# Performance work log

Measured on AMD Instinct MI355X. Metric: run time of the kernel, lower is better.

The kernel has to match this reference:

```python
import jax, jax.numpy as jnp
import numpy as np

N = 50000      # nodes
E = 800000     # edges (avg degree 16)
F_IN = 128
H = 128        # hidden_channels
C = 10         # num_classes
S = 5          # Chebyshev order K
B = 8          # graphs in batch


def setup_inputs() -> dict:
    key = jax.random.key(0)
    ks = jax.random.split(key, 9)
    x = jax.random.normal(ks[0], (N, F_IN), jnp.float32)
    edge_index = jax.random.randint(ks[1], (2, E), 0, N, dtype=jnp.int64)
    batch = jnp.sort(jax.random.randint(ks[2], (N,), 0, B, dtype=jnp.int64))
    lambda_max = 2.0 * jnp.ones((B,), jnp.float32)
    W1 = jax.random.normal(ks[3], (S, F_IN, H), jnp.float32) * 0.05
    b1 = jax.random.normal(ks[4], (H,), jnp.float32) * 0.05
    W2 = jax.random.normal(ks[5], (S, H, H), jnp.float32) * 0.05
    b2 = jax.random.normal(ks[6], (H,), jnp.float32) * 0.05
    Wlin = jax.random.normal(ks[7], (H, C), jnp.float32) * 0.05
    blin = jax.random.normal(ks[8], (C,), jnp.float32) * 0.05
    return {"x": x, "edge_index": edge_index, "batch": batch,
            "lambda_max": lambda_max, "W1": W1, "b1": b1,
            "W2": W2, "b2": b2, "Wlin": Wlin, "blin": blin}


def _cheb_conv(x, row, col, w_edge, diag, W, b):
    # scaled Laplacian matvec: L_hat v = scatter(w_edge * v[col] -> row) + diag * v
    def Lhat(v):
        msg = v[col] * w_edge[:, None]                       # [E, d]
        return jax.ops.segment_sum(msg, row, num_segments=N) + diag[:, None] * v

    Tx0 = x
    out = Tx0 @ W[0]
    Tx1 = Lhat(Tx0)
    out = out + Tx1 @ W[1]
    for k in range(2, W.shape[0]):                           # Chebyshev recurrence
        Tx2 = 2.0 * Lhat(Tx1) - Tx0
        out = out + Tx2 @ W[k]
        Tx0, Tx1 = Tx1, Tx2
    return out + b


def reference(x, edge_index, batch, lambda_max, W1, b1, W2, b2, Wlin, blin):
    row, col = edge_index[0], edge_index[1]
    # sym-normalized Laplacian L = I - D^{-1/2} A D^{-1/2}; L_hat = 2L/lambda_max - I
    deg = jax.ops.segment_sum(jnp.ones((E,), x.dtype), row, num_segments=N)
    dis = jnp.where(deg > 0, jax.lax.rsqrt(jnp.maximum(deg, 1e-12)), 0.0)
    lam_e = lambda_max[batch[row]]                           # per-edge lambda_max
    w_edge = -2.0 * dis[row] * dis[col] / lam_e              # off-diagonal of L_hat
    diag = 2.0 / lambda_max[batch] - 1.0                     # diagonal of L_hat per node

    h = jax.nn.relu(_cheb_conv(x, row, col, w_edge, diag, W1, b1))
    h = jax.nn.relu(_cheb_conv(h, row, col, w_edge, diag, W2, b2))

    # global_mean_pool over batch assignment
    sums = jax.ops.segment_sum(h, batch, num_segments=B)     # [B, H]
    counts = jax.ops.segment_sum(jnp.ones((N, 1), h.dtype), batch, num_segments=B)
    pooled = sums / jnp.maximum(counts, 1.0)
    return pooled @ Wlin + blin                              # [B, C] logits (softmax unused in forward)
```

## Files before the change

kernel.cpp:

```cpp
#include <hip/hip_runtime.h>
#include <hip/hip_bf16.h>
#include <stdint.h>

typedef __attribute__((ext_vector_type(8))) short bf16x8;
typedef __attribute__((ext_vector_type(4))) float f32x4;

__device__ __forceinline__ float bf16lo_to_f(uint32_t u) { return __uint_as_float(u << 16); }
__device__ __forceinline__ float bf16hi_to_f(uint32_t u) { return __uint_as_float(u & 0xffff0000u); }
__device__ __forceinline__ uint16_t f_to_bf16(float f) {
    uint32_t u = __float_as_uint(f);
    uint32_t r = u + 0x7fff + ((u >> 16) & 1);
    return (uint16_t)(r >> 16);
}


#define BINCH 4096

__global__ void __launch_bounds__(256) k_bhist(const int* __restrict__ row,
                                               int* __restrict__ bhist, int E) {
    __shared__ int sh[256];
    int t = threadIdx.x;
    sh[t] = 0;
    __syncthreads();
    int stride = gridDim.x * blockDim.x;
    for (int e = blockIdx.x * blockDim.x + t; e < E; e += stride)
        atomicAdd(&sh[row[e] >> 8], 1);
    __syncthreads();
    if (sh[t]) atomicAdd(&bhist[t], sh[t]);
}

__global__ void k_bscan(const int* __restrict__ bhist, int* __restrict__ gbase,
                        int* __restrict__ gcur, float* __restrict__ mS, int nbk, int N) {
    __shared__ int sh[256];
    int t = threadIdx.x;
    int v = t < nbk ? bhist[t] : 0;
    sh[t] = v;
    __syncthreads();
    for (int o = 1; o < 256; o <<= 1) {
        int u = (t >= o) ? sh[t - o] : 0;
        __syncthreads();
        sh[t] += u;
        __syncthreads();
    }
    gbase[t] = sh[t] - v;
    gcur[t] = sh[t] - v;
    if (t == 255) gbase[256] = sh[255];
    if (t < 5) mS[(size_t)t * (N + 1) + N] = 0.f;
}

__global__ void __launch_bounds__(256) k_bin(const int* __restrict__ row,
        const int* __restrict__ col, int* __restrict__ gcur,
        uint32_t* __restrict__ bout, int E) {
    __shared__ uint32_t stage[BINCH];
    __shared__ int hist[256], hscan[256], hcur[256], gofs[256];
    int t = threadIdx.x;
    int e0 = blockIdx.x * BINCH;
    int ecnt = min(BINCH, E - e0);
    hist[t] = 0;
    __syncthreads();
    for (int i = t; i < ecnt; i += 256)
        atomicAdd(&hist[row[e0 + i] >> 8], 1);
    __syncthreads();
    int v = hist[t];
    hscan[t] = v;
    __syncthreads();
    for (int o = 1; o < 256; o <<= 1) {
        int u = (t >= o) ? hscan[t - o] : 0;
        __syncthreads();
        hscan[t] += u;
        __syncthreads();
    }
    hcur[t] = hscan[t] - v;
    __syncthreads();
    for (int i = t; i < ecnt; i += 256) {
        int r = row[e0 + i];
        int p = atomicAdd(&hcur[r >> 8], 1);
        stage[p] = (uint32_t)(r & 255) | ((uint32_t)col[e0 + i] << 8);
    }
    __syncthreads();
    if (v > 0) gofs[t] = atomicAdd(&gcur[t], v);
    __syncthreads();
    for (int i = t; i < ecnt; i += 256) {
        int lo = 0, hi = 255;
        while (lo < hi) { int mid = (lo + hi) >> 1; if (hscan[mid] > i) hi = mid; else lo = mid + 1; }
        int b = lo;
        int local = i - (hscan[b] - hist[b]);
        bout[gofs[b] + local] = stage[i];
    }
}

__global__ void __launch_bounds__(256) k_deg2(const uint32_t* __restrict__ bout,
        const int* __restrict__ gbase, int* __restrict__ deg,
        int* __restrict__ psum, int N) {
    __shared__ int cnt[256];
    __shared__ int red[256];
    int t = threadIdx.x, b = blockIdx.x;
    cnt[t] = 0;
    __syncthreads();
    int s = gbase[b], epos = gbase[b + 1];
    for (int i = s + t; i < epos; i += 256)
        atomicAdd(&cnt[bout[i] & 255], 1);
    __syncthreads();
    int n = b * 256 + t;
    int d = cnt[t];
    if (n < N) deg[n] = d;
    red[t] = (n < N) ? ((d + 7) & ~7) : 0;
    __syncthreads();
    for (int o = 128; o > 0; o >>= 1) {
        if (t < o) red[t] += red[t + o];
        __syncthreads();
    }
    if (t == 0) psum[b] = red[0];
}

__global__ void k_scanp(const int* __restrict__ psum, int* __restrict__ poff,
                        int* __restrict__ offs, int nb, int N) {
    __shared__ int sh[256];
    int t = threadIdx.x;
    int per = (nb + 255) >> 8;
    int base = t * per;
    int s = 0;
    for (int i = 0; i < per; i++) { int idx = base + i; if (idx < nb) s += psum[idx]; }
    sh[t] = s;
    __syncthreads();
    for (int o = 1; o < 256; o <<= 1) {
        int u = (t >= o) ? sh[t - o] : 0;
        __syncthreads();
        sh[t] += u;
        __syncthreads();
    }
    int run = sh[t] - s;
    for (int i = 0; i < per; i++) {
        int idx = base + i;
        if (idx < nb) { poff[idx] = run; run += psum[idx]; }
    }
    if (t == 255) offs[N] = sh[255];
}

__global__ void k_offs(const int* __restrict__ deg, const int* __restrict__ poff,
                       int* __restrict__ offs,
                       const int* __restrict__ batch, const float* __restrict__ lam,
                       float* __restrict__ dis, float* __restrict__ diag, int N) {
    __shared__ int sh[256];
    int t = threadIdx.x;
    int idx = blockIdx.x * 256 + t;
    int d = idx < N ? deg[idx] : 0;
    int v = (d + 7) & ~7;
    sh[t] = v;
    __syncthreads();
    for (int o = 1; o < 256; o <<= 1) {
        int u = (t >= o) ? sh[t - o] : 0;
        __syncthreads();
        sh[t] += u;
        __syncthreads();
    }
    if (idx < N) {
        offs[idx] = poff[blockIdx.x] + sh[t] - v;
        dis[idx] = d > 0 ? rsqrtf((float)d) : 0.f;
        diag[idx] = 2.f / lam[batch[idx]] - 1.f;
    }
}

__global__ void __launch_bounds__(256) k_csr2(const uint32_t* __restrict__ bout,
        const int* __restrict__ gbase, const int* __restrict__ offs,
        uint16_t* __restrict__ csr, int N) {
    __shared__ int cur[256];
    int t = threadIdx.x, b = blockIdx.x;
    int n = b * 256 + t;
    int o0 = n < N ? offs[n] : 0;
    cur[t] = o0;
    __syncthreads();
    int s = gbase[b], epos = gbase[b + 1];
    for (int i = s + t; i < epos; i += 256) {
        uint32_t v = bout[i];
        int p = atomicAdd(&cur[v & 255], 1);
        csr[p] = (uint16_t)(v >> 8);
    }
    __syncthreads();
    if (n < N) {
        int e = cur[t];
        int pe = o0 + ((e - o0 + 7) & ~7);
        for (int p = e; p < pe; p++) csr[p] = (uint16_t)N;
    }
}

__global__ void k_prepw(const float* __restrict__ W1, uint16_t* __restrict__ Wt1,
                        const float* __restrict__ W2, uint16_t* __restrict__ Wt2) {
    int i = blockIdx.x * blockDim.x + threadIdx.x;
    const float* W = W1; uint16_t* Wt = Wt1;
    if (i >= 128 * 640) { i -= 128 * 640; W = W2; Wt = Wt2; }
    int o = i / 640, kk = i % 640;
    Wt[(size_t)o * 640 + kk] = f_to_bf16(W[(size_t)kk * 128 + o]);
}

__global__ void __launch_bounds__(256) k_castx(const float* __restrict__ x,
        uint16_t* __restrict__ Txb, int8_t* __restrict__ Txq,
        const float* __restrict__ dis, float* __restrict__ mS,
        float* __restrict__ scq, int N) {
    int n = (blockIdx.x * blockDim.x + threadIdx.x) >> 6;
    int lane = threadIdx.x & 63;
    if (n >= N) return;
    float2 v = ((const float2*)x)[(size_t)n * 64 + lane];
    uint32_t p = (uint32_t)f_to_bf16(v.x) | ((uint32_t)f_to_bf16(v.y) << 16);
    __builtin_nontemporal_store(p, &((uint32_t*)Txb)[(size_t)n * 320 + lane]);
    float m = fmaxf(fabsf(v.x), fabsf(v.y));
    for (int o = 1; o < 64; o <<= 1) m = fmaxf(m, __shfl_xor(m, o));
    float inv = m > 0.f ? 127.f / m : 0.f;
    int qx = (int)rintf(v.x * inv), qy = (int)rintf(v.y * inv);
    uint16_t qp = (uint16_t)((qx & 0xff) | ((qy & 0xff) << 8));
    *(uint16_t*)(Txq + (size_t)n * 640 + 2 * lane) = qp;
    if (lane == 0) {
        float sc = m > 0.f ? m * (1.f / 127.f) : 0.f;
        mS[n] = sc * dis[n];
        scq[n] = sc;
    }
}

__global__ void __launch_bounds__(256) k_lhat(
        int8_t* __restrict__ Txq, uint16_t* __restrict__ Txb,
        const int* __restrict__ offs, const uint16_t* __restrict__ csr,
        const float* __restrict__ diag, const float* __restrict__ dis,
        float* __restrict__ mS, float* __restrict__ scq, int N,
        int src, int dst, int prev, float alpha, int use_prev) {
    int n = (blockIdx.x * blockDim.x + threadIdx.x) >> 6;
    int lane = threadIdx.x & 63;
    if (n >= N) return;
    int beg = offs[n], end = offs[n + 1];
    float dgn = diag[n], dn = dis[n];
    float aS = -alpha * dn * (dgn + 1.0f);
    const float* mSrc = mS + (size_t)src * (N + 1);
    const int8_t* qbase = Txq + src * 128 + 2 * lane;
    float ax = 0.f, ay = 0.f;
    for (int e = beg; e < end; e += 8) {
        uint4 cw = *(const uint4*)(csr + e);
        int cc[8] = { (int)(cw.x & 0xffff), (int)(cw.x >> 16),
                      (int)(cw.y & 0xffff), (int)(cw.y >> 16),
                      (int)(cw.z & 0xffff), (int)(cw.z >> 16),
                      (int)(cw.w & 0xffff), (int)(cw.w >> 16) };
        float mm[8];
        uint16_t qv[8];
#pragma unroll
        for (int u = 0; u < 8; u++) mm[u] = mSrc[cc[u]];
#pragma unroll
        for (int u = 0; u < 8; u++)
            qv[u] = *(const uint16_t*)(qbase + (size_t)cc[u] * 640);
#pragma unroll
        for (int u = 0; u < 8; u++) {
            float f = aS * mm[u];
            ax = fmaf(f, (float)(int)(int8_t)(qv[u] & 0xff), ax);
            ay = fmaf(f, (float)(int)(int8_t)(qv[u] >> 8), ay);
        }
    }
    {
        uint16_t qsv = *(const uint16_t*)(Txq + (size_t)n * 640 + src * 128 + 2 * lane);
        float ad = alpha * dgn * scq[(size_t)src * (N + 1) + n];
        ax = fmaf(ad, (float)(int)(int8_t)(qsv & 0xff), ax);
        ay = fmaf(ad, (float)(int)(int8_t)(qsv >> 8), ay);
    }
    if (use_prev) {
        uint16_t qpv = *(const uint16_t*)(Txq + (size_t)n * 640 + prev * 128 + 2 * lane);
        float sp = scq[(size_t)prev * (N + 1) + n];
        ax = fmaf(-sp, (float)(int)(int8_t)(qpv & 0xff), ax);
        ay = fmaf(-sp, (float)(int)(int8_t)(qpv >> 8), ay);
    }
    uint32_t outv = (uint32_t)f_to_bf16(ax) | ((uint32_t)f_to_bf16(ay) << 16);
    __builtin_nontemporal_store(outv, &((uint32_t*)Txb)[(size_t)n * 320 + dst * 64 + lane]);
    float m = fmaxf(fabsf(ax), fabsf(ay));
    for (int o = 1; o < 64; o <<= 1) m = fmaxf(m, __shfl_xor(m, o));
    float inv = m > 0.f ? 127.f / m : 0.f;
    int qx = (int)rintf(ax * inv), qy = (int)rintf(ay * inv);
    uint16_t qp = (uint16_t)((qx & 0xff) | ((qy & 0xff) << 8));
    *(uint16_t*)(Txq + (size_t)n * 640 + dst * 128 + 2 * lane) = qp;
    if (lane == 0) {
        float sc = m > 0.f ? m * (1.f / 127.f) : 0.f;
        mS[(size_t)dst * (N + 1) + n] = sc * dn;
        scq[(size_t)dst * (N + 1) + n] = sc;
    }
}

#define BM 128
#define BK 64
#define LDT 72
#define LDC 132

__global__ void __launch_bounds__(256) k_gemm(
        const uint16_t* __restrict__ A, int lda,
        const uint16_t* __restrict__ Bt,
        const float* __restrict__ bias,
        uint16_t* __restrict__ out, int ldo,
        uint16_t* __restrict__ out2b,
        int8_t* __restrict__ out2q,
        const float* __restrict__ dis, float* __restrict__ mS,
        float* __restrict__ scq,
        int M, int Kdim) {
    __shared__ uint16_t smem[BM * LDT + 128 * LDT];
    uint16_t* As = smem;
    uint16_t* Bs = smem + BM * LDT;
    uint16_t* Ct = smem;
    int t = threadIdx.x;
    int w = t >> 6, lane = t & 63;
    int row0 = blockIdx.x * BM;
    int mrow = (w >> 1) * 64, ncol = (w & 1) * 64;

    int ar[4], akc[4];
#pragma unroll
    for (int rep = 0; rep < 4; rep++) {
        int d = rep * 256 + t;
        ar[rep] = d >> 3; akc[rep] = d & 7;
    }

    f32x4 acc[4][4];
#pragma unroll
    for (int i = 0; i < 4; i++)
#pragma unroll
        for (int j = 0; j < 4; j++) acc[i][j] = (f32x4){0.f, 0.f, 0.f, 0.f};

    bf16x8 pa[4], pb[4];
#pragma unroll
    for (int rep = 0; rep < 4; rep++) {
        int grow = row0 + ar[rep];
        bf16x8 va = {0, 0, 0, 0, 0, 0, 0, 0};
        if (grow < M) va = *(const bf16x8*)(A + (size_t)grow * lda + akc[rep] * 8);
        pa[rep] = va;
        pb[rep] = *(const bf16x8*)(Bt + (size_t)ar[rep] * Kdim + akc[rep] * 8);
    }

    for (int k0 = 0; k0 < Kdim; k0 += BK) {
#pragma unroll
        for (int rep = 0; rep < 4; rep++) {
            *(bf16x8*)(&As[ar[rep] * LDT + akc[rep] * 8]) = pa[rep];
            *(bf16x8*)(&Bs[ar[rep] * LDT + akc[rep] * 8]) = pb[rep];
        }
        __syncthreads();
        int kn = k0 + BK;
        if (kn < Kdim) {
#pragma unroll
            for (int rep = 0; rep < 4; rep++) {
                int grow = row0 + ar[rep];
                bf16x8 va = {0, 0, 0, 0, 0, 0, 0, 0};
                if (grow < M) va = *(const bf16x8*)(A + (size_t)grow * lda + kn + akc[rep] * 8);
                pa[rep] = va;
                pb[rep] = *(const bf16x8*)(Bt + (size_t)ar[rep] * Kdim + kn + akc[rep] * 8);
            }
        }
#pragma unroll
        for (int ks = 0; ks < BK; ks += 32) {
            bf16x8 af[4], bfr[4];
#pragma unroll
            for (int i = 0; i < 4; i++) {
                int r = mrow + i * 16 + (lane & 15);
                af[i] = *(const bf16x8*)(&As[r * LDT + ks + (lane >> 4) * 8]);
            }
#pragma unroll
            for (int j = 0; j < 4; j++) {
                int c = ncol + j * 16 + (lane & 15);
                bfr[j] = *(const bf16x8*)(&Bs[c * LDT + ks + (lane >> 4) * 8]);
            }
#pragma unroll
            for (int i = 0; i < 4; i++)
#pragma unroll
                for (int j = 0; j < 4; j++)
                    acc[i][j] = __builtin_amdgcn_mfma_f32_16x16x32_bf16(af[i], bfr[j], acc[i][j], 0, 0, 0);
        }
        __syncthreads();
    }

#pragma unroll
    for (int j = 0; j < 4; j++) {
        int c = ncol + j * 16 + (lane & 15);
        float bv = bias[c];
#pragma unroll
        for (int i = 0; i < 4; i++) {
            int rloc = mrow + i * 16 + (lane >> 4) * 4;
#pragma unroll
            for (int r = 0; r < 4; r++) {
                float v = acc[i][j][r] + bv;
                v = v > 0.f ? v : 0.f;
                Ct[(rloc + r) * LDC + c] = f_to_bf16(v);
            }
        }
    }
    __syncthreads();
#pragma unroll
    for (int rep = 0; rep < 8; rep++) {
        int d = rep * 256 + t;
        int r = d >> 4, c8 = (d & 15) * 8;
        int grow = row0 + r;
        if (grow < M) {
            bf16x8 v = *(const bf16x8*)(&Ct[r * LDC + c8]);
            if (out)   *(bf16x8*)(out + (size_t)grow * ldo + c8) = v;
            if (out2b) *(bf16x8*)(out2b + (size_t)grow * 640 + c8) = v;
        }
    }
    if (out2q) {
        int r = t >> 1, half = t & 1;
        int grow = row0 + r;
        float vmax = 0.f;
        for (int j = 0; j < 32; j++) {
            uint32_t u = *(const uint32_t*)(&Ct[r * LDC + half * 64 + j * 2]);
            vmax = fmaxf(vmax, fmaxf(fabsf(bf16lo_to_f(u)), fabsf(bf16hi_to_f(u))));
        }
        vmax = fmaxf(vmax, __shfl_xor(vmax, 1));
        if (grow < M) {
            float inv = vmax > 0.f ? 127.f / vmax : 0.f;
            for (int j0 = 0; j0 < 16; j0++) {
                uint32_t u0 = *(const uint32_t*)(&Ct[r * LDC + half * 64 + j0 * 4]);
                uint32_t u1 = *(const uint32_t*)(&Ct[r * LDC + half * 64 + j0 * 4 + 2]);
                int q0 = (int)rintf(bf16lo_to_f(u0) * inv);
                int q1 = (int)rintf(bf16hi_to_f(u0) * inv);
                int q2 = (int)rintf(bf16lo_to_f(u1) * inv);
                int q3 = (int)rintf(bf16hi_to_f(u1) * inv);
                uint32_t pk = (q0 & 0xff) | ((q1 & 0xff) << 8) |
                              ((q2 & 0xff) << 16) | ((uint32_t)(q3 & 0xff) << 24);
                *(uint32_t*)(out2q + (size_t)grow * 640 + half * 64 + j0 * 4) = pk;
            }
            if (half == 0) {
                float sc = vmax > 0.f ? vmax * (1.f / 127.f) : 0.f;
                mS[grow] = sc * dis[grow];
                scq[grow] = sc;
            }
        }
    }
}

__global__ void __launch_bounds__(128) k_pool(const uint16_t* __restrict__ h,
        const int* __restrict__ batch, float* __restrict__ pooled, int N, int CH) {
    int f = threadIdx.x;
    int n0 = blockIdx.x * CH;
    if (n0 >= N) return;
    int n1 = min(n0 + CH, N);
    float acc = 0.f;
    int cur = batch[n0];
    for (int n = n0; n < n1; ++n) {
        int b = batch[n];
        if (b != cur) { atomicAdd(&pooled[cur * 128 + f], acc); acc = 0.f; cur = b; }
        acc += __uint_as_float(((uint32_t)h[(size_t)n * 128 + f]) << 16);
    }
    atomicAdd(&pooled[cur * 128 + f], acc);
}

__global__ void k_final(const float* __restrict__ pooled, const int* __restrict__ batch,
                        const float* __restrict__ Wlin, const float* __restrict__ blin,
                        float* __restrict__ out, int N, int B_, int C_) {
    __shared__ int cnt[64];
    int t = threadIdx.x;
    if (t < B_) {
        auto lb = [&](int v) {
            int lo = 0, hi = N;
            while (lo < hi) {
                int mid = (lo + hi) >> 1;
                if (batch[mid] < v) lo = mid + 1; else hi = mid;
            }
            return lo;
        };
        cnt[t] = lb(t + 1) - lb(t);
    }
    __syncthreads();
    if (t < B_ * C_) {
        int b = t / C_, c = t % C_;
        float inv = 1.f / fmaxf((float)cnt[b], 1.f);
        float acc = blin[c];
        for (int f = 0; f < 128; ++f) acc += pooled[b * 128 + f] * inv * Wlin[f * C_ + c];
        out[t] = acc;
    }
}

extern "C" void kernel_launch(void* const* d_in, const int* in_sizes, int n_in,
                              void* d_out, int out_size, void* d_ws, size_t ws_size,
                              hipStream_t stream) {
    const float* x    = (const float*)d_in[0];
    const int*   edge = (const int*)d_in[1];
    const int*   batch= (const int*)d_in[2];
    const float* lam  = (const float*)d_in[3];
    const float* W1   = (const float*)d_in[4];
    const float* b1   = (const float*)d_in[5];
    const float* W2   = (const float*)d_in[6];
    const float* b2   = (const float*)d_in[7];
    const float* Wlin = (const float*)d_in[8];
    const float* blin = (const float*)d_in[9];
    const int E  = in_sizes[1] / 2;
    const int N  = in_sizes[2];
    const int B_ = in_sizes[3];
    const int* row = edge;
    const int* col = edge + E;

    char* ws = (char*)d_ws;
    size_t off = 0;
    auto take = [&](size_t bytes) -> char* {
        char* p = ws + off;
        off = (off + bytes + 255) & ~(size_t)255;
        return p;
    };
    uint16_t* Txb    = (uint16_t*)take((size_t)N * 640 * 2);
    int8_t*   Txq    = (int8_t*)take((size_t)(N + 1) * 640);
    uint16_t* h      = (uint16_t*)take((size_t)N * 128 * 2);
    uint16_t* csr    = (uint16_t*)take(((size_t)E + 8 * (size_t)N) * 2);
    uint32_t* bout   = (uint32_t*)take((size_t)E * 4);
    float*    mS     = (float*)take((size_t)5 * (N + 1) * 4);
    float*    scq    = (float*)take((size_t)5 * (N + 1) * 4);
    int*      deg    = (int*)take((size_t)N * 4);
    int*      offs   = (int*)take((size_t)(N + 1) * 4);
    float*    dis    = (float*)take((size_t)N * 4);
    float*    diag   = (float*)take((size_t)N * 4);
    uint16_t* Wt1    = (uint16_t*)take((size_t)128 * 640 * 2);
    uint16_t* Wt2    = (uint16_t*)take((size_t)128 * 640 * 2);
    float*    pooled = (float*)take((size_t)B_ * 128 * 4);
    int*      bhist  = (int*)take(257 * 4);
    int*      gbase  = (int*)take(257 * 4);
    int*      gcur   = (int*)take(257 * 4);
    const int nb = (N + 255) / 256;
    int*      psum   = (int*)take((size_t)nb * 4);
    int*      poff   = (int*)take((size_t)nb * 4);

    hipMemsetAsync(pooled, 0, (size_t)B_ * 128 * 4, stream);
    hipMemsetAsync(bhist, 0, 257 * 4, stream);

    k_bhist<<<112, 256, 0, stream>>>(row, bhist, E);
    k_bscan<<<1, 256, 0, stream>>>(bhist, gbase, gcur, mS, nb, N);
    k_bin<<<(E + BINCH - 1) / BINCH, 256, 0, stream>>>(row, col, gcur, bout, E);
    k_deg2<<<nb, 256, 0, stream>>>(bout, gbase, deg, psum, N);
    k_scanp<<<1, 256, 0, stream>>>(psum, poff, offs, nb, N);
    k_offs<<<nb, 256, 0, stream>>>(deg, poff, offs, batch, lam, dis, diag, N);
    k_csr2<<<nb, 256, 0, stream>>>(bout, gbase, offs, csr, N);
    k_prepw<<<(2 * 128 * 640) / 256, 256, 0, stream>>>(W1, Wt1, W2, Wt2);
    k_castx<<<(N + 3) / 4, 256, 0, stream>>>(x, Txb, Txq, dis, mS, scq, N);

    const int lblocks = (N + 3) / 4;
    const int gblocks = (N + BM - 1) / BM;

    k_lhat<<<lblocks, 256, 0, stream>>>(Txq, Txb, offs, csr, diag, dis, mS, scq, N, 0, 1, 0, 1.f, 0);
    k_lhat<<<lblocks, 256, 0, stream>>>(Txq, Txb, offs, csr, diag, dis, mS, scq, N, 1, 2, 0, 2.f, 1);
    k_lhat<<<lblocks, 256, 0, stream>>>(Txq, Txb, offs, csr, diag, dis, mS, scq, N, 2, 3, 1, 2.f, 1);
    k_lhat<<<lblocks, 256, 0, stream>>>(Txq, Txb, offs, csr, diag, dis, mS, scq, N, 3, 4, 2, 2.f, 1);
    k_gemm<<<gblocks, 256, 0, stream>>>(Txb, 640, Wt1, b1,
                                        (uint16_t*)nullptr, 128, Txb, Txq, dis, mS, scq, N, 640);

    k_lhat<<<lblocks, 256, 0, stream>>>(Txq, Txb, offs, csr, diag, dis, mS, scq, N, 0, 1, 0, 1.f, 0);
    k_lhat<<<lblocks, 256, 0, stream>>>(Txq, Txb, offs, csr, diag, dis, mS, scq, N, 1, 2, 0, 2.f, 1);
    k_lhat<<<lblocks, 256, 0, stream>>>(Txq, Txb, offs, csr, diag, dis, mS, scq, N, 2, 3, 1, 2.f, 1);
    k_lhat<<<lblocks, 256, 0, stream>>>(Txq, Txb, offs, csr, diag, dis, mS, scq, N, 3, 4, 2, 2.f, 1);
    k_gemm<<<gblocks, 256, 0, stream>>>(Txb, 640, Wt2, b2, h, 128,
                                        (uint16_t*)nullptr, (int8_t*)nullptr, dis, mS, scq, N, 640);

    k_pool<<<(N + 127) / 128, 128, 0, stream>>>(h, batch, pooled, N, 128);
    k_final<<<1, 128, 0, stream>>>(pooled, batch, Wlin, blin, (float*)d_out, N, B_, 10);
}
```

Measured before the change: 513.5 us.

## Fuse mean-pool into GEMM epilogue and fold prefix scan into offsets kernel

The second GEMM now accumulates per-graph feature sums directly from its shared-memory output tile with atomics, removing the h buffer write and the separate pooling kernel. The single-block partial-sum scan kernel is removed; each offsets block instead reduces the psum entries before it in shared memory. The two memsets are merged into one, relying on pooled and bhist being adjacent in the workspace. This cuts launches and global traffic, but it assumes at most 256 partial blocks and a specific workspace layout.

```diff
diff --git a/kernel.cpp b/kernel.cpp
--- a/kernel.cpp
+++ b/kernel.cpp
@@ -113,37 +113,23 @@
     if (t == 0) psum[b] = red[0];
 }
 
-__global__ void k_scanp(const int* __restrict__ psum, int* __restrict__ poff,
-                        int* __restrict__ offs, int nb, int N) {
-    __shared__ int sh[256];
-    int t = threadIdx.x;
-    int per = (nb + 255) >> 8;
-    int base = t * per;
-    int s = 0;
-    for (int i = 0; i < per; i++) { int idx = base + i; if (idx < nb) s += psum[idx]; }
-    sh[t] = s;
-    __syncthreads();
-    for (int o = 1; o < 256; o <<= 1) {
-        int u = (t >= o) ? sh[t - o] : 0;
-        __syncthreads();
-        sh[t] += u;
-        __syncthreads();
-    }
-    int run = sh[t] - s;
-    for (int i = 0; i < per; i++) {
-        int idx = base + i;
-        if (idx < nb) { poff[idx] = run; run += psum[idx]; }
-    }
-    if (t == 255) offs[N] = sh[255];
-}
-
-__global__ void k_offs(const int* __restrict__ deg, const int* __restrict__ poff,
+__global__ void k_offs(const int* __restrict__ deg, const int* __restrict__ psum,
                        int* __restrict__ offs,
                        const int* __restrict__ batch, const float* __restrict__ lam,
-                       float* __restrict__ dis, float* __restrict__ diag, int N) {
+                       float* __restrict__ dis, float* __restrict__ diag,
+                       int N, int nb) {
+    __shared__ int pre[256];
     __shared__ int sh[256];
-    int t = threadIdx.x;
-    int idx = blockIdx.x * 256 + t;
+    int t = threadIdx.x, b = blockIdx.x;
+    pre[t] = (t < b) ? psum[t] : 0;
+    __syncthreads();
+    for (int o = 128; o > 0; o >>= 1) {
+        if (t < o) pre[t] += pre[t + o];
+        __syncthreads();
+    }
+    int base = pre[0];
+    __syncthreads();
+    int idx = b * 256 + t;
     int d = idx < N ? deg[idx] : 0;
     int v = (d + 7) & ~7;
     sh[t] = v;
@@ -155,10 +141,11 @@
         __syncthreads();
     }
     if (idx < N) {
-        offs[idx] = poff[blockIdx.x] + sh[t] - v;
+        offs[idx] = base + sh[t] - v;
         dis[idx] = d > 0 ? rsqrtf((float)d) : 0.f;
         diag[idx] = 2.f / lam[batch[idx]] - 1.f;
     }
+    if (b == nb - 1 && t == 255) offs[N] = base + sh[255];
 }
 
 __global__ void __launch_bounds__(256) k_csr2(const uint32_t* __restrict__ bout,
@@ -287,11 +274,12 @@
         const uint16_t* __restrict__ A, int lda,
         const uint16_t* __restrict__ Bt,
         const float* __restrict__ bias,
-        uint16_t* __restrict__ out, int ldo,
         uint16_t* __restrict__ out2b,
         int8_t* __restrict__ out2q,
         const float* __restrict__ dis, float* __restrict__ mS,
         float* __restrict__ scq,
+        float* __restrict__ pooled,
+        const int* __restrict__ batch,
         int M, int Kdim) {
     __shared__ uint16_t smem[BM * LDT + 128 * LDT];
     uint16_t* As = smem;
@@ -381,15 +369,17 @@
         }
     }
     __syncthreads();
-#pragma unroll
-    for (int rep = 0; rep < 8; rep++) {
-        int d = rep * 256 + t;
-        int r = d >> 4, c8 = (d & 15) * 8;
-        int grow = row0 + r;
-        if (grow < M) {
-            bf16x8 v = *(const bf16x8*)(&Ct[r * LDC + c8]);
-            if (out)   *(bf16x8*)(out + (size_t)grow * ldo + c8) = v;
-            if (out2b) *(bf16x8*)(out2b + (size_t)grow * 640 + c8) = v;
+
+    if (out2b) {
+#pragma unroll
+        for (int rep = 0; rep < 8; rep++) {
+            int d = rep * 256 + t;
+            int r = d >> 4, c8 = (d & 15) * 8;
+            int grow = row0 + r;
+            if (grow < M) {
+                bf16x8 v = *(const bf16x8*)(&Ct[r * LDC + c8]);
+                *(bf16x8*)(out2b + (size_t)grow * 640 + c8) = v;
+            }
         }
     }
     if (out2q) {
@@ -421,22 +411,22 @@
             }
         }
     }
-}
-
-__global__ void __launch_bounds__(128) k_pool(const uint16_t* __restrict__ h,
-        const int* __restrict__ batch, float* __restrict__ pooled, int N, int CH) {
-    int f = threadIdx.x;
-    int n0 = blockIdx.x * CH;
-    if (n0 >= N) return;
-    int n1 = min(n0 + CH, N);
-    float acc = 0.f;
-    int cur = batch[n0];
-    for (int n = n0; n < n1; ++n) {
-        int b = batch[n];
-        if (b != cur) { atomicAdd(&pooled[cur * 128 + f], acc); acc = 0.f; cur = b; }
-        acc += __uint_as_float(((uint32_t)h[(size_t)n * 128 + f]) << 16);
-    }
-    atomicAdd(&pooled[cur * 128 + f], acc);
+    if (pooled) {
+        int f = t & 127, r0 = (t >> 7) * 64;
+        float accp = 0.f;
+        int curb = -1;
+        for (int r = r0; r < r0 + 64; ++r) {
+            int grow = row0 + r;
+            if (grow >= M) break;
+            int b = batch[grow];
+            if (b != curb) {
+                if (curb >= 0) atomicAdd(&pooled[curb * 128 + f], accp);
+                accp = 0.f; curb = b;
+            }
+            accp += __uint_as_float(((uint32_t)Ct[r * LDC + f]) << 16);
+        }
+        if (curb >= 0) atomicAdd(&pooled[curb * 128 + f], accp);
+    }
 }
 
 __global__ void k_final(const float* __restrict__ pooled, const int* __restrict__ batch,
@@ -493,7 +483,6 @@
     };
     uint16_t* Txb    = (uint16_t*)take((size_t)N * 640 * 2);
     int8_t*   Txq    = (int8_t*)take((size_t)(N + 1) * 640);
-    uint16_t* h      = (uint16_t*)take((size_t)N * 128 * 2);
     uint16_t* csr    = (uint16_t*)take(((size_t)E + 8 * (size_t)N) * 2);
     uint32_t* bout   = (uint32_t*)take((size_t)E * 4);
     float*    mS     = (float*)take((size_t)5 * (N + 1) * 4);
@@ -510,17 +499,14 @@
     int*      gcur   = (int*)take(257 * 4);
     const int nb = (N + 255) / 256;
     int*      psum   = (int*)take((size_t)nb * 4);
-    int*      poff   = (int*)take((size_t)nb * 4);
-
-    hipMemsetAsync(pooled, 0, (size_t)B_ * 128 * 4, stream);
-    hipMemsetAsync(bhist, 0, 257 * 4, stream);
+
+    hipMemsetAsync(pooled, 0, (size_t)B_ * 128 * 4 + 257 * 4, stream);
 
     k_bhist<<<112, 256, 0, stream>>>(row, bhist, E);
     k_bscan<<<1, 256, 0, stream>>>(bhist, gbase, gcur, mS, nb, N);
     k_bin<<<(E + BINCH - 1) / BINCH, 256, 0, stream>>>(row, col, gcur, bout, E);
     k_deg2<<<nb, 256, 0, stream>>>(bout, gbase, deg, psum, N);
-    k_scanp<<<1, 256, 0, stream>>>(psum, poff, offs, nb, N);
-    k_offs<<<nb, 256, 0, stream>>>(deg, poff, offs, batch, lam, dis, diag, N);
+    k_offs<<<nb, 256, 0, stream>>>(deg, psum, offs, batch, lam, dis, diag, N, nb);
     k_csr2<<<nb, 256, 0, stream>>>(bout, gbase, offs, csr, N);
     k_prepw<<<(2 * 128 * 640) / 256, 256, 0, stream>>>(W1, Wt1, W2, Wt2);
     k_castx<<<(N + 3) / 4, 256, 0, stream>>>(x, Txb, Txq, dis, mS, scq, N);
@@ -533,15 +519,16 @@
     k_lhat<<<lblocks, 256, 0, stream>>>(Txq, Txb, offs, csr, diag, dis, mS, scq, N, 2, 3, 1, 2.f, 1);
     k_lhat<<<lblocks, 256, 0, stream>>>(Txq, Txb, offs, csr, diag, dis, mS, scq, N, 3, 4, 2, 2.f, 1);
     k_gemm<<<gblocks, 256, 0, stream>>>(Txb, 640, Wt1, b1,
-                                        (uint16_t*)nullptr, 128, Txb, Txq, dis, mS, scq, N, 640);
+                                        Txb, Txq, dis, mS, scq,
+                                        (float*)nullptr, batch, N, 640);
 
     k_lhat<<<lblocks, 256, 0, stream>>>(Txq, Txb, offs, csr, diag, dis, mS, scq, N, 0, 1, 0, 1.f, 0);
     k_lhat<<<lblocks, 256, 0, stream>>>(Txq, Txb, offs, csr, diag, dis, mS, scq, N, 1, 2, 0, 2.f, 1);
     k_lhat<<<lblocks, 256, 0, stream>>>(Txq, Txb, offs, csr, diag, dis, mS, scq, N, 2, 3, 1, 2.f, 1);
     k_lhat<<<lblocks, 256, 0, stream>>>(Txq, Txb, offs, csr, diag, dis, mS, scq, N, 3, 4, 2, 2.f, 1);
-    k_gemm<<<gblocks, 256, 0, stream>>>(Txb, 640, Wt2, b2, h, 128,
-                                        (uint16_t*)nullptr, (int8_t*)nullptr, dis, mS, scq, N, 640);
-
-    k_pool<<<(N + 127) / 128, 128, 0, stream>>>(h, batch, pooled, N, 128);
+    k_gemm<<<gblocks, 256, 0, stream>>>(Txb, 640, Wt2, b2,
+                                        (uint16_t*)nullptr, (int8_t*)nullptr, dis, mS, scq,
+                                        pooled, batch, N, 640);
+
     k_final<<<1, 128, 0, stream>>>(pooled, batch, Wlin, blin, (float*)d_out, N, B_, 10);
 }
```

Result: faster. 481.7 us, median of 2 (-6.2%).
